# Kernel optimization log

Hardware: AMD Instinct MI355X
Metric: run time of the kernel (lower is better)

## Reference

```python
import jax, jax.numpy as jnp
import numpy as np

NUM_EXPERT = 16
IN_FEAT = 1024
OUT_FEAT = 1024
BATCH = 8192


def setup_inputs() -> dict:
    key = jax.random.key(0)
    k_inp, k_gate, k_w = jax.random.split(key, 3)
    inp = jax.random.normal(k_inp, (BATCH, IN_FEAT), dtype=jnp.float32)
    gate = jax.random.randint(k_gate, (BATCH,), 0, NUM_EXPERT, dtype=jnp.int32)
    # nn.Linear default init: uniform(-1/sqrt(in_feat), 1/sqrt(in_feat))
    bound = 1.0 / np.sqrt(IN_FEAT)
    weight = jax.random.uniform(
        k_w, (NUM_EXPERT, OUT_FEAT, IN_FEAT), dtype=jnp.float32,
        minval=-bound, maxval=bound)
    return {"inp": inp, "gate": gate, "weight": weight}


def reference(inp, gate, weight):
    # o[t] = weight[gate[t]] @ inp[t]
    # Loop over the (small, fixed) expert axis via lax.scan; each step does a
    # dense [B, in] @ [in, out] GEMM and keeps rows routed to that expert.
    num_expert, out_feat, _ = weight.shape
    batch = inp.shape[0]

    def body(o, xs):
        i, w = xs  # w: [out_feat, in_feat]
        y = inp @ w.T  # [batch, out_feat]
        sel = (gate == i)[:, None]
        return jnp.where(sel, y, o), None

    o0 = jnp.zeros((batch, out_feat), dtype=inp.dtype)
    o, _ = jax.lax.scan(body, o0, (jnp.arange(num_expert), weight))
    return o
```

## Files before the change

### kernel.cpp

```cpp
#include <hip/hip_runtime.h>
#include <hip/hip_bf16.h>

#define NE    16
#define KDIM  1024
#define NDIM  1024
#define BATCH 8192
#define TM    128
#define TN    64
#define MAXT  96

typedef __attribute__((ext_vector_type(8))) short short8;
typedef __attribute__((ext_vector_type(4))) float floatx4;
typedef unsigned short ushort_t;

#define O_CNT  0
#define O_TG0  256
#define O_TE   1024
#define O_TEND 2048
#define O_POS  4096
#define O_TOK  36864
#define O_PA   73728
#define O_W    17113088
#define WS_REQ 50667520

#define GLOAD_LDS(gp, lp) __builtin_amdgcn_global_load_lds( \
    (const __attribute__((address_space(1))) unsigned int*)(gp), \
    (__attribute__((address_space(3))) unsigned int*)(lp), 16, 0, 0)

__device__ __forceinline__ unsigned int pk2bf(float x, float y) {
    __hip_bfloat162 h = __float22bfloat162_rn(make_float2(x, y));
    unsigned int u;
    __builtin_memcpy(&u, &h, 4);
    return u;
}


__global__ void zero_k(int* cnt) {
    if (threadIdx.x < NE) cnt[threadIdx.x] = 0;
}

__global__ void hist_k(const int* __restrict__ gate, int* cnt, int* pos) {
    int t = blockIdx.x * blockDim.x + threadIdx.x;
    if (t < BATCH) pos[t] = atomicAdd(&cnt[gate[t]], 1);
}

__global__ __launch_bounds__(256, 8) void prep_k(
        const float* __restrict__ inp, const float* __restrict__ wgt,
        const int* __restrict__ gate, const int* __restrict__ pos,
        const int* __restrict__ cnt, ushort_t* __restrict__ pA,
        ushort_t* __restrict__ pW, int* __restrict__ tok,
        int* __restrict__ tg0, int* __restrict__ te, int* __restrict__ tend) {
    __shared__ int ntot;
    const int b = blockIdx.x, tid = threadIdx.x;
    if (b < 2048) {
        const int col = (tid & 127) * 8;
        const int half = tid >> 7;
        int g[2]; float4 v0[2], v1[2];
        #pragma unroll
        for (int p = 0; p < 2; ++p) {
            int t = b * 4 + p * 2 + half;
            int e = gate[t];
            int off = 0;
            #pragma unroll
            for (int k = 0; k < NE; ++k) off += (k < e) ? cnt[k] : 0;
            g[p] = off + pos[t];
            v0[p] = *(const float4*)&inp[(size_t)t * KDIM + col];
            v1[p] = *(const float4*)&inp[(size_t)t * KDIM + col + 4];
        }
        #pragma unroll
        for (int p = 0; p < 2; ++p) {
            uint4 u = make_uint4(pk2bf(v0[p].x, v0[p].y), pk2bf(v0[p].z, v0[p].w),
                                 pk2bf(v1[p].x, v1[p].y), pk2bf(v1[p].z, v1[p].w));
            *(uint4*)&pA[(size_t)g[p] * KDIM + col] = u;
            if (col == 0) tok[g[p]] = b * 4 + p * 2 + half;
        }
        size_t base = (size_t)b * 8192 + tid * 8;
        float4 va[4], vb[4];
        #pragma unroll
        for (int i = 0; i < 4; ++i) {
            va[i] = *(const float4*)&wgt[base + i * 2048];
            vb[i] = *(const float4*)&wgt[base + i * 2048 + 4];
        }
        #pragma unroll
        for (int i = 0; i < 4; ++i) {
            uint4 u = make_uint4(pk2bf(va[i].x, va[i].y), pk2bf(va[i].z, va[i].w),
                                 pk2bf(vb[i].x, vb[i].y), pk2bf(vb[i].z, vb[i].w));
            *(uint4*)&pW[base + i * 2048] = u;
        }
    } else {
        if (tid < NE) {
            int o = 0, ts = 0;
            for (int j = 0; j < NE; ++j) {
                int c = cnt[j];
                if (j < tid) { o += c; ts += (c + TM - 1) / TM; }
            }
            int c = cnt[tid];
            if (tid == NE - 1) ntot = ts + (c + TM - 1) / TM;
            int nt = ts;
            for (int r = 0; r < c; r += TM) {
                int r0 = (r + TM <= c) ? r : (c > TM ? c - TM : 0);
                tg0[nt] = o + r0; te[nt] = tid; tend[nt] = o + c; ++nt;
            }
        }
        __syncthreads();
        for (int i = ntot + tid; i < MAXT; i += 256) {
            tg0[i] = 0; te[i] = 0; tend[i] = 0;
        }
    }
}

__global__ __launch_bounds__(256, 5) void moe_gemm4_k(
        const ushort_t* __restrict__ pA, const ushort_t* __restrict__ pW,
        const int* __restrict__ tg0, const int* __restrict__ teArr,
        const int* __restrict__ tend, const int* __restrict__ tok,
        float* __restrict__ out) {
    const int y   = blockIdx.y;
    const int g0  = tg0[y];
    const int end = tend[y];
    if (g0 >= end) return;
    const int e    = teArr[y];
    const int out0 = blockIdx.x * TN;

    __shared__ ushort_t As[TM][64];
    __shared__ ushort_t Bs[TN][64];
    __shared__ int tok_s[TM];

    const int tid = threadIdx.x;
    if (tid < TM) tok_s[tid] = tok[g0 + tid];

    const int wave = tid >> 6, lane = tid & 63;
    const int wm = (wave >> 1) * 64;
    const int wn = (wave & 1) * 32;
    const int quad = lane >> 4, l16 = lane & 15;

    const ushort_t* Ab = pA + (size_t)g0 * KDIM;
    const ushort_t* Bb = pW + (size_t)e * (KDIM * NDIM) + (size_t)out0 * KDIM;

    floatx4 acc[4][2] = {};
    const int slotw = wave * 64 + lane;

    for (int k0 = 0; k0 < KDIM; k0 += 64) {
        #pragma unroll
        for (int i = 0; i < 4; ++i) {
            int slot = i * 256 + slotw;
            int row = slot >> 3;
            int kc = (slot & 7) ^ (row & 7);
            GLOAD_LDS(Ab + (size_t)row * KDIM + k0 + kc * 8,
                      (ushort_t*)As + (size_t)(i * 256 + wave * 64) * 8);
        }
        #pragma unroll
        for (int i = 0; i < 2; ++i) {
            int slot = i * 256 + slotw;
            int row = slot >> 3;
            int kc = (slot & 7) ^ (row & 7);
            GLOAD_LDS(Bb + (size_t)row * KDIM + k0 + kc * 8,
                      (ushort_t*)Bs + (size_t)(i * 256 + wave * 64) * 8);
        }
        __syncthreads();
        #pragma unroll
        for (int s = 0; s < 2; ++s) {
            short8 a[4], b[2];
            #pragma unroll
            for (int i = 0; i < 4; ++i) {
                int r = wm + i * 16 + l16;
                a[i] = *(const short8*)&As[r][((s * 4 + quad) ^ (r & 7)) * 8];
            }
            #pragma unroll
            for (int j = 0; j < 2; ++j) {
                int r = wn + j * 16 + l16;
                b[j] = *(const short8*)&Bs[r][((s * 4 + quad) ^ (r & 7)) * 8];
            }
            #pragma unroll
            for (int mi = 0; mi < 4; ++mi)
                #pragma unroll
                for (int nj = 0; nj < 2; ++nj)
                    acc[mi][nj] = __builtin_amdgcn_mfma_f32_16x16x32_bf16(
                        a[mi], b[nj], acc[mi][nj], 0, 0, 0);
        }
        __syncthreads();
    }

    #pragma unroll
    for (int mi = 0; mi < 4; ++mi) {
        #pragma unroll
        for (int r = 0; r < 4; ++r) {
            int lrow = wm + mi * 16 + quad * 4 + r;
            if (g0 + lrow < end) {
                int t = tok_s[lrow];
                float* orow = out + (size_t)t * NDIM + out0 + wn + l16;
                #pragma unroll
                for (int nj = 0; nj < 2; ++nj)
                    orow[nj * 16] = acc[mi][nj][r];
            }
        }
    }
}

#define LDW 20
__global__ void bin_tokens_k(const int* __restrict__ gate, int* cnt, int* idx) {
    int t = blockIdx.x * blockDim.x + threadIdx.x;
    if (t < BATCH) {
        int e = gate[t];
        int p = atomicAdd(&cnt[e], 1);
        idx[e * BATCH + p] = t;
    }
}

__global__ __launch_bounds__(256) void moe_gemm_k(
        const float* __restrict__ inp, const float* __restrict__ wgt,
        const int* __restrict__ cnt, const int* __restrict__ idx,
        float* __restrict__ out) {
    const int e = blockIdx.z;
    const int n_e = cnt[e];
    const int row0 = blockIdx.y * TM;
    if (row0 >= n_e) return;
    const int out0 = blockIdx.x * 128;
    __shared__ unsigned int As[TM * LDW];
    __shared__ unsigned int Bs[TM * LDW];
    __shared__ int tok_s[TM];
    const int tid = threadIdx.x;
    if (tid < TM) {
        int g = row0 + tid;
        tok_s[tid] = (g < n_e) ? idx[e * BATCH + g] : -1;
    }
    const int wave = tid >> 6, lane = tid & 63;
    const int wm = (wave >> 1) * 64, wn = (wave & 1) * 64;
    const int quad = lane >> 4, l16 = lane & 15;
    floatx4 acc[4][4] = {};
    const int cg = (tid & 7) * 4;
    const int rbase = tid >> 3;
    const float* wbase = wgt + (size_t)e * KDIM * NDIM;
    for (int k0 = 0; k0 < KDIM; k0 += 32) {
        __syncthreads();
        #pragma unroll
        for (int p = 0; p < 4; ++p) {
            int row = p * 32 + rbase;
            int t = tok_s[row];
            float4 va = make_float4(0.f, 0.f, 0.f, 0.f);
            if (t >= 0) va = *(const float4*)&inp[(size_t)t * KDIM + k0 + cg];
            As[row * LDW + (cg >> 1)]     = pk2bf(va.x, va.y);
            As[row * LDW + (cg >> 1) + 1] = pk2bf(va.z, va.w);
            float4 vb = *(const float4*)&wbase[(size_t)(out0 + row) * KDIM + k0 + cg];
            Bs[row * LDW + (cg >> 1)]     = pk2bf(vb.x, vb.y);
            Bs[row * LDW + (cg >> 1) + 1] = pk2bf(vb.z, vb.w);
        }
        __syncthreads();
        short8 a[4], b[4];
        #pragma unroll
        for (int i = 0; i < 4; ++i)
            a[i] = *(const short8*)&As[(wm + i * 16 + l16) * LDW + quad * 4];
        #pragma unroll
        for (int i = 0; i < 4; ++i)
            b[i] = *(const short8*)&Bs[(wn + i * 16 + l16) * LDW + quad * 4];
        #pragma unroll
        for (int mi = 0; mi < 4; ++mi)
            #pragma unroll
            for (int ni = 0; ni < 4; ++ni)
                acc[mi][ni] = __builtin_amdgcn_mfma_f32_16x16x32_bf16(
                    a[mi], b[ni], acc[mi][ni], 0, 0, 0);
    }
    #pragma unroll
    for (int mi = 0; mi < 4; ++mi) {
        #pragma unroll
        for (int r = 0; r < 4; ++r) {
            int lrow = wm + mi * 16 + quad * 4 + r;
            int t = tok_s[lrow];
            if (t >= 0) {
                float* orow = out + (size_t)t * NDIM + out0 + wn + l16;
                #pragma unroll
                for (int ni = 0; ni < 4; ++ni)
                    orow[ni * 16] = acc[mi][ni][r];
            }
        }
    }
}

extern "C" void kernel_launch(void* const* d_in, const int* in_sizes, int n_in,
                              void* d_out, int out_size, void* d_ws, size_t ws_size,
                              hipStream_t stream) {
    const float* inp  = (const float*)d_in[0];
    const int*   gate = (const int*)d_in[1];
    const float* wgt  = (const float*)d_in[2];
    float*       out  = (float*)d_out;
    char* w = (char*)d_ws;

    if (ws_size >= WS_REQ) {
        int* cnt  = (int*)(w + O_CNT);
        int* tg0  = (int*)(w + O_TG0);
        int* te   = (int*)(w + O_TE);
        int* tend = (int*)(w + O_TEND);
        int* pos  = (int*)(w + O_POS);
        int* tok  = (int*)(w + O_TOK);
        ushort_t* pA = (ushort_t*)(w + O_PA);
        ushort_t* pW = (ushort_t*)(w + O_W);

        zero_k<<<1, 64, 0, stream>>>(cnt);
        hist_k<<<BATCH / 256, 256, 0, stream>>>(gate, cnt, pos);
        prep_k<<<2048 + 1, 256, 0, stream>>>(inp, wgt, gate, pos, cnt,
                                             pA, pW, tok, tg0, te, tend);
        dim3 grid(NDIM / TN, MAXT, 1);
        moe_gemm4_k<<<grid, 256, 0, stream>>>(pA, pW, tg0, te, tend, tok, out);
    } else {
        int* cnt = (int*)d_ws;
        int* idx = cnt + NE;
        zero_k<<<1, 64, 0, stream>>>(cnt);
        bin_tokens_k<<<BATCH / 256, 256, 0, stream>>>(gate, cnt, idx);
        dim3 grid(NDIM / 128, BATCH / TM, NE);
        moe_gemm_k<<<grid, 256, 0, stream>>>(inp, wgt, cnt, idx, out);
    }
}
```

Measured before the change: 194.6 us.

## Fuse weight fp32-to-bf16 conversion into the MoE GEMM B-tile load

The separate prep pass that converted all expert weights to bf16 in a workspace buffer is removed. The GEMM now loads fp32 weight tiles into registers, converts them to bf16 and stores them to LDS itself, replacing the async global-to-LDS load for B. This avoids writing and re-reading a 32MB bf16 weight copy and shrinks the workspace. In exchange, each GEMM block re-reads and re-converts fp32 weights, which doubles B traffic per tile. The B loads also pass through registers instead of going directly to LDS, which may hurt latency hiding and register pressure.

```diff
diff --git a/kernel.cpp b/kernel.cpp
--- a/kernel.cpp
+++ b/kernel.cpp
@@ -20,8 +20,7 @@
 #define O_POS  4096
 #define O_TOK  36864
 #define O_PA   73728
-#define O_W    17113088
-#define WS_REQ 50667520
+#define WS_REQ 17113088
 
 #define GLOAD_LDS(gp, lp) __builtin_amdgcn_global_load_lds( \
     (const __attribute__((address_space(1))) unsigned int*)(gp), \
@@ -45,10 +44,9 @@
 }
 
 __global__ __launch_bounds__(256, 8) void prep_k(
-        const float* __restrict__ inp, const float* __restrict__ wgt,
-        const int* __restrict__ gate, const int* __restrict__ pos,
-        const int* __restrict__ cnt, ushort_t* __restrict__ pA,
-        ushort_t* __restrict__ pW, int* __restrict__ tok,
+        const float* __restrict__ inp, const int* __restrict__ gate,
+        const int* __restrict__ pos, const int* __restrict__ cnt,
+        ushort_t* __restrict__ pA, int* __restrict__ tok,
         int* __restrict__ tg0, int* __restrict__ te, int* __restrict__ tend) {
     __shared__ int ntot;
     const int b = blockIdx.x, tid = threadIdx.x;
@@ -74,19 +72,6 @@
             *(uint4*)&pA[(size_t)g[p] * KDIM + col] = u;
             if (col == 0) tok[g[p]] = b * 4 + p * 2 + half;
         }
-        size_t base = (size_t)b * 8192 + tid * 8;
-        float4 va[4], vb[4];
-        #pragma unroll
-        for (int i = 0; i < 4; ++i) {
-            va[i] = *(const float4*)&wgt[base + i * 2048];
-            vb[i] = *(const float4*)&wgt[base + i * 2048 + 4];
-        }
-        #pragma unroll
-        for (int i = 0; i < 4; ++i) {
-            uint4 u = make_uint4(pk2bf(va[i].x, va[i].y), pk2bf(va[i].z, va[i].w),
-                                 pk2bf(vb[i].x, vb[i].y), pk2bf(vb[i].z, vb[i].w));
-            *(uint4*)&pW[base + i * 2048] = u;
-        }
     } else {
         if (tid < NE) {
             int o = 0, ts = 0;
@@ -109,8 +94,8 @@
     }
 }
 
-__global__ __launch_bounds__(256, 5) void moe_gemm4_k(
-        const ushort_t* __restrict__ pA, const ushort_t* __restrict__ pW,
+__global__ __launch_bounds__(256, 5) void moe_gemm5_k(
+        const ushort_t* __restrict__ pA, const float* __restrict__ wgt,
         const int* __restrict__ tg0, const int* __restrict__ teArr,
         const int* __restrict__ tend, const int* __restrict__ tok,
         float* __restrict__ out) {
@@ -134,12 +119,22 @@
     const int quad = lane >> 4, l16 = lane & 15;
 
     const ushort_t* Ab = pA + (size_t)g0 * KDIM;
-    const ushort_t* Bb = pW + (size_t)e * (KDIM * NDIM) + (size_t)out0 * KDIM;
+    const float*    Bw = wgt + ((size_t)e * NDIM + out0) * KDIM;
 
     floatx4 acc[4][2] = {};
     const int slotw = wave * 64 + lane;
 
     for (int k0 = 0; k0 < KDIM; k0 += 64) {
+        float4 bv[2][2];
+        #pragma unroll
+        for (int i = 0; i < 2; ++i) {
+            int slot = i * 256 + slotw;
+            int row = slot >> 3;
+            int kc = (slot & 7) ^ (row & 7);
+            const float* src = Bw + (size_t)row * KDIM + k0 + kc * 8;
+            bv[i][0] = *(const float4*)src;
+            bv[i][1] = *(const float4*)(src + 4);
+        }
         #pragma unroll
         for (int i = 0; i < 4; ++i) {
             int slot = i * 256 + slotw;
@@ -151,10 +146,11 @@
         #pragma unroll
         for (int i = 0; i < 2; ++i) {
             int slot = i * 256 + slotw;
-            int row = slot >> 3;
-            int kc = (slot & 7) ^ (row & 7);
-            GLOAD_LDS(Bb + (size_t)row * KDIM + k0 + kc * 8,
-                      (ushort_t*)Bs + (size_t)(i * 256 + wave * 64) * 8);
+            uint4 u = make_uint4(pk2bf(bv[i][0].x, bv[i][0].y),
+                                 pk2bf(bv[i][0].z, bv[i][0].w),
+                                 pk2bf(bv[i][1].x, bv[i][1].y),
+                                 pk2bf(bv[i][1].z, bv[i][1].w));
+            *(uint4*)((ushort_t*)Bs + (size_t)slot * 8) = u;
         }
         __syncthreads();
         #pragma unroll
@@ -292,14 +288,13 @@
         int* pos  = (int*)(w + O_POS);
         int* tok  = (int*)(w + O_TOK);
         ushort_t* pA = (ushort_t*)(w + O_PA);
-        ushort_t* pW = (ushort_t*)(w + O_W);
 
         zero_k<<<1, 64, 0, stream>>>(cnt);
         hist_k<<<BATCH / 256, 256, 0, stream>>>(gate, cnt, pos);
-        prep_k<<<2048 + 1, 256, 0, stream>>>(inp, wgt, gate, pos, cnt,
-                                             pA, pW, tok, tg0, te, tend);
+        prep_k<<<2048 + 1, 256, 0, stream>>>(inp, gate, pos, cnt,
+                                             pA, tok, tg0, te, tend);
         dim3 grid(NDIM / TN, MAXT, 1);
-        moe_gemm4_k<<<grid, 256, 0, stream>>>(pA, pW, tg0, te, tend, tok, out);
+        moe_gemm5_k<<<grid, 256, 0, stream>>>(pA, wgt, tg0, te, tend, tok, out);
     } else {
         int* cnt = (int*)d_ws;
         int* idx = cnt + NE;
```

Result: no change. 192.8 us (-0.9%).
